# Kernel tuning notes

Measured on AMD Instinct MI355X. Metric: run time of the kernel, lower is better.

The kernel has to match this reference:

```python
import jax, jax.numpy as jnp
import numpy as np

EPS = 1e-5  # pyg LayerNorm default eps


def _graph_ln(x):
    # pyg.nn.norm.LayerNorm(affine=False), default mode='graph', batch=None:
    # normalizes over ALL elements of the tensor (x - x.mean()) / x.std(unbiased=False)
    m = x.mean()
    v = jnp.mean((x - m) ** 2)
    return (x - m) * jax.lax.rsqrt(v + EPS)


def _cheb_conv(x, row, col, w, W, b):
    # ChebConv, normalization='sym', lambda_max=2 => scaled Laplacian
    # L_hat = L - I = -D^{-1/2} A D^{-1/2} (self-loops removed, weighted)
    # x: [B,N,C_in], row/col: [E], w: [E], W: [K,C_in,C_out], b: [C_out]
    N = x.shape[1]
    w = jnp.where(row == col, 0.0, w)  # remove_self_loops
    deg = jnp.zeros((N,), x.dtype).at[row].add(w)
    dinv = jnp.where(deg > 0, jax.lax.rsqrt(jnp.maximum(deg, 1e-12)), 0.0)
    norm = -(dinv[row] * w * dinv[col])  # [E]

    def prop(t):  # out[i] += norm_e * t[j] for edge (j=row -> i=col)
        msg = norm[None, :, None] * t[:, row, :]  # [B,E,C]
        return jnp.zeros_like(t).at[:, col, :].add(msg)

    Tx0 = x
    out = jnp.einsum('bnc,cd->bnd', Tx0, W[0])
    Tx1 = prop(x)
    out = out + jnp.einsum('bnc,cd->bnd', Tx1, W[1])
    for k in range(2, W.shape[0]):
        Tx2 = 2.0 * prop(Tx1) - Tx0
        out = out + jnp.einsum('bnc,cd->bnd', Tx2, W[k])
        Tx0, Tx1 = Tx1, Tx2
    return out + b


def setup_inputs() -> dict:
    key = jax.random.key(0)
    ks = jax.random.split(key, 8)
    B, N, C, E, L, K = 8, 2048, 256, 32768, 3, 3
    node_feature = jax.random.normal(ks[0], (B, N, C), dtype=jnp.float32)
    edge_index = jax.random.randint(ks[1], (L, 2, E), 0, N)
    edge_weight = jax.random.uniform(ks[2], (L, E), dtype=jnp.float32)
    s = 1.0 / np.sqrt(C)
    cheb_w = jax.random.normal(ks[3], (L, K, C, C), dtype=jnp.float32) * s
    cheb_b = jnp.zeros((L, C), dtype=jnp.float32)
    mlp_w = jax.random.normal(ks[4], (L, C, C), dtype=jnp.float32) * s
    mlp_b = jax.random.normal(ks[5], (L, C), dtype=jnp.float32) * 0.01
    return {"node_feature": node_feature, "edge_weight": edge_weight,
            "cheb_w": cheb_w, "cheb_b": cheb_b, "mlp_w": mlp_w,
            "mlp_b": mlp_b, "edge_index": edge_index}


def reference(node_feature, edge_weight, cheb_w, cheb_b, mlp_w, mlp_b, edge_index):
    h = node_feature  # [B,N,C]
    L = cheb_w.shape[0]
    for l in range(L):
        h_res = h
        hn = _graph_ln(h)
        hc = _cheb_conv(hn, edge_index[l, 0], edge_index[l, 1],
                        edge_weight[l], cheb_w[l], cheb_b[l])
        h = hc + h_res
        h_res = h
        hn = _graph_ln(h)
        hm = jax.nn.gelu(jnp.einsum('bnc,cd->bnd', hn, mlp_w[l]) + mlp_b[l],
                         approximate=False)  # dropout is identity at inference
        h = hm + h_res
    return h.mean(axis=1)  # [B,C]
```

## Files before the change

### kernel.cpp

```cpp
#include <hip/hip_runtime.h>

#define BATCH   8
#define NNODE   2048
#define CH      256
#define NEDGE   32768
#define NLAYER  3
#define MROWS   (NNODE*BATCH)
#define KCAT    (3*CH)
#define NTOT    (MROWS*CH)

typedef _Float16 half8 __attribute__((ext_vector_type(8)));
typedef _Float16 half4 __attribute__((ext_vector_type(4)));
typedef float    f32x4 __attribute__((ext_vector_type(4)));

#define OFF_ACAT   ((size_t)0)
#define OFF_HF     ((size_t)25165824)
#define OFF_WT     ((size_t)33554432)
#define OFF_MT     ((size_t)34734080)
#define OFF_PARTA  ((size_t)35127296)
#define OFF_PARTB  ((size_t)35135488)
#define OFF_CS     ((size_t)35143680)
#define OFF_CSM    ((size_t)35152896)
#define OFF_DEG    ((size_t)35155968)
#define OFF_CNT    ((size_t)35180544)
#define OFF_ELIST  ((size_t)35205120)
#define OFF_NORM   ((size_t)36777984)
#define OFF_R1     ((size_t)37171200)
#define OFF_R2     ((size_t)37195776)

__device__ __forceinline__ void async_lds16(const void* g, void* l) {
  __builtin_amdgcn_global_load_lds((const __attribute__((address_space(1))) void*)g,
                                   (__attribute__((address_space(3))) void*)l, 16, 0, 0);
}

__global__ __launch_bounds__(256) void k_init(const float* __restrict__ x,
                                              _Float16* __restrict__ Acat,
                                              float2* __restrict__ part,
                                              const float* __restrict__ cheb_w,
                                              const float* __restrict__ mlp_w,
                                              _Float16* __restrict__ Wt,
                                              _Float16* __restrict__ Mt,
                                              float* __restrict__ deg,
                                              unsigned int* __restrict__ count,
                                              float* __restrict__ r1) {
  __shared__ float rs[512];
  __shared__ _Float16 lt[64][72];
  const int blk = blockIdx.x, t = threadIdx.x;
  if (blk < 1024) {
    int tid = blk*256 + t;
    float s = 0.f, s2 = 0.f;
    for (int i = tid; i < NTOT/4; i += 1024*256) {
      int c4 = i & 63, b = (i >> 6) & 7, n = i >> 9;
      float4 v = ((const float4*)x)[((b*NNODE + n) << 6) + c4];
      half4 o; o[0]=(_Float16)v.x; o[1]=(_Float16)v.y; o[2]=(_Float16)v.z; o[3]=(_Float16)v.w;
      *(half4*)&Acat[(size_t)(i >> 6)*KCAT + c4*4] = o;
      s  += v.x + v.y + v.z + v.w;
      s2 += v.x*v.x + v.y*v.y + v.z*v.z + v.w*v.w;
    }
    rs[t] = s; rs[256+t] = s2; __syncthreads();
    for (int o = 128; o > 0; o >>= 1) {
      if (t < o) { rs[t] += rs[t+o]; rs[256+t] += rs[256+t+o]; }
      __syncthreads();
    }
    if (t == 0) part[blk] = make_float2(rs[0], rs[256]);
  } else if (blk < 1048) {
    int i = (blk - 1024)*256 + t;
    if (i < NLAYER*NNODE) { deg[i] = 0.f; count[i] = 0u; r1[i] = 0.f; }
  } else {
    const int tile = blk - 1048;
    const int rr = t >> 4, c4 = t & 15;
    if (tile < 144) {
      const int l = tile / 48, rem = tile % 48;
      const int kk = rem / 16, q = rem % 16, ci = q >> 2, ni = q & 3;
      const float4* W  = (const float4*)cheb_w + ((size_t)((l*3 + kk)*CH + ci*64))*64 + ni*16;
      const float4* W2 = (const float4*)cheb_w + ((size_t)((l*3 + 2 )*CH + ci*64))*64 + ni*16;
      #pragma unroll
      for (int p = 0; p < 4; ++p) {
        const int r = p*16 + rr;
        float4 v = W[(size_t)r*64 + c4];
        if (kk == 0) {
          float4 v2 = W2[(size_t)r*64 + c4];
          v.x -= v2.x; v.y -= v2.y; v.z -= v2.z; v.w -= v2.w;
        } else if (kk == 2) {
          v.x *= 2.f; v.y *= 2.f; v.z *= 2.f; v.w *= 2.f;
        }
        lt[c4*4+0][r] = (_Float16)v.x; lt[c4*4+1][r] = (_Float16)v.y;
        lt[c4*4+2][r] = (_Float16)v.z; lt[c4*4+3][r] = (_Float16)v.w;
      }
      __syncthreads();
      const int nr = t >> 2, ch2 = t & 3;
      #pragma unroll
      for (int pp = 0; pp < 2; ++pp) {
        const int ch = ch2 + pp*4;
        half8 v = *(const half8*)&lt[nr][ch*8];
        *(half8*)&Wt[((size_t)(l*CH + ni*64 + nr))*KCAT + kk*256 + ci*64 + ch*8] = v;
      }
    } else {
      const int m = tile - 144;
      const int l = m / 16, q = m % 16, ci = q >> 2, ni = q & 3;
      const float4* W = (const float4*)mlp_w + ((size_t)(l*CH + ci*64))*64 + ni*16;
      #pragma unroll
      for (int p = 0; p < 4; ++p) {
        const int r = p*16 + rr;
        float4 v = W[(size_t)r*64 + c4];
        lt[c4*4+0][r] = (_Float16)v.x; lt[c4*4+1][r] = (_Float16)v.y;
        lt[c4*4+2][r] = (_Float16)v.z; lt[c4*4+3][r] = (_Float16)v.w;
      }
      __syncthreads();
      const int nr = t >> 2, ch2 = t & 3;
      #pragma unroll
      for (int pp = 0; pp < 2; ++pp) {
        const int ch = ch2 + pp*4;
        half8 v = *(const half8*)&lt[nr][ch*8];
        *(half8*)&Mt[((size_t)(l*CH + ni*64 + nr))*CH + ci*64 + ch*8] = v;
      }
    }
  }
}

__global__ __launch_bounds__(256) void k_edge_scatter(const int* __restrict__ ei,
                                                      const float* __restrict__ ew,
                                                      float* deg, unsigned int* count,
                                                      unsigned int* elist) {
  int i = blockIdx.x*256 + threadIdx.x;
  if (i >= NLAYER*NEDGE) return;
  int l = i / NEDGE, e = i % NEDGE;
  const int* rows = ei + l*2*NEDGE;
  const int* cols = rows + NEDGE;
  int r = rows[e], c = cols[e];
  float w = (r == c) ? 0.f : ew[i];
  atomicAdd(&deg[l*NNODE + r], w);
  unsigned int slot = atomicAdd(&count[l*NNODE + c], 1u);
  if (slot < 64u) elist[(size_t)(l*NNODE + c)*64 + slot] = (unsigned int)e;
}

__global__ __launch_bounds__(256) void k_edge_norm(const int* __restrict__ ei,
                                                   const float* __restrict__ ew,
                                                   const float* __restrict__ deg,
                                                   float* __restrict__ norm,
                                                   float* __restrict__ r1) {
  int i = blockIdx.x*256 + threadIdx.x;
  if (i >= NLAYER*NEDGE) return;
  int l = i / NEDGE, e = i % NEDGE;
  const int* rows = ei + l*2*NEDGE;
  const int* cols = rows + NEDGE;
  int r = rows[e], c = cols[e];
  float w = (r == c) ? 0.f : ew[i];
  float dr = deg[l*NNODE + r], dc = deg[l*NNODE + c];
  float ir = dr > 0.f ? rsqrtf(fmaxf(dr, 1e-12f)) : 0.f;
  float ic = dc > 0.f ? rsqrtf(fmaxf(dc, 1e-12f)) : 0.f;
  float nm = -(ir * w * ic);
  norm[i] = nm;
  atomicAdd(&r1[l*NNODE + c], nm);
}

template<int SRC_OFF, int DST_OFF, int AUX>
__global__ __launch_bounds__(256) void k_prop(_Float16* __restrict__ Acat,
                                              const int* __restrict__ rows,
                                              const float* __restrict__ nrm,
                                              const unsigned int* __restrict__ count,
                                              const unsigned int* __restrict__ el,
                                              const int* __restrict__ ei,
                                              const float* __restrict__ norm_all,
                                              const unsigned int* __restrict__ cnt_all,
                                              const unsigned int* __restrict__ el_all,
                                              const float* __restrict__ r1,
                                              float* __restrict__ r2,
                                              const _Float16* __restrict__ Wt,
                                              const _Float16* __restrict__ Mt,
                                              float* __restrict__ cs,
                                              float* __restrict__ csM,
                                              float* __restrict__ out_zero) {
  const int blk = blockIdx.x, t = threadIdx.x;
  if (!AUX || blk < 4096) {
    const int b = blk & 7, dgrp = blk >> 3;
    const int w = t >> 6, lane = t & 63;
    const int dst = dgrp*4 + w;
    unsigned int c = count[dst]; if (c > 64u) c = 64u;
    int srcv = 0; float nmv = 0.f;
    if (lane < (int)c) {
      unsigned int e = el[(size_t)dst*64 + lane];
      srcv = rows[e]; nmv = nrm[e];
    }
    float a0 = 0.f, a1 = 0.f, a2 = 0.f, a3 = 0.f;
    const _Float16* base = Acat + SRC_OFF + b*KCAT + lane*4;
    #define PROP_STEP(i)                                                            \
      {                                                                             \
        int   src = __builtin_amdgcn_readlane(srcv, (i));                           \
        int   nbi = __builtin_amdgcn_readlane(__builtin_bit_cast(int, nmv), (i));   \
        float nm  = __builtin_bit_cast(float, nbi);                                 \
        half4 v = *(const half4*)&base[(size_t)src*8*KCAT];                         \
        a0 += nm*(float)v[0]; a1 += nm*(float)v[1];                                 \
        a2 += nm*(float)v[2]; a3 += nm*(float)v[3];                                 \
      }
    unsigned int i = 0;
    for (; i + 4 <= c; i += 4) { PROP_STEP(i) PROP_STEP(i+1) PROP_STEP(i+2) PROP_STEP(i+3) }
    for (; i < c; ++i) { PROP_STEP(i) }
    #undef PROP_STEP
    half4 o; o[0] = (_Float16)a0; o[1] = (_Float16)a1; o[2] = (_Float16)a2; o[3] = (_Float16)a3;
    *(half4*)&Acat[(size_t)(dst*8 + b)*KCAT + DST_OFF + lane*4] = o;
  } else {
    const int tile = blk - 4096;
    if (tile < 24) {
      int i = tile*256 + t, l = i / NNODE;
      const int* rw = ei + l*2*NEDGE;
      unsigned int c = cnt_all[i]; if (c > 64u) c = 64u;
      const unsigned int* elp = el_all + (size_t)i*64;
      float s = 0.f;
      for (unsigned int j = 0; j < c; ++j) {
        unsigned int e = elp[j];
        s += norm_all[l*NEDGE + e] * r1[l*NNODE + rw[e]];
      }
      r2[i] = s;
    } else if (tile < 33) {
      int idx = tile - 24, l = idx / 3, kk = idx % 3, n = t;
      const half8* row = (const half8*)&Wt[((size_t)(l*CH + n))*KCAT + kk*256];
      float s = 0.f;
      #pragma unroll 4
      for (int j = 0; j < 32; ++j) {
        half8 v = row[j];
        s += (float)v[0]+(float)v[1]+(float)v[2]+(float)v[3]
           + (float)v[4]+(float)v[5]+(float)v[6]+(float)v[7];
      }
      cs[(l*3 + kk)*CH + n] = s;
    } else if (tile < 36) {
      int l = tile - 33, n = t;
      const half8* row = (const half8*)&Mt[((size_t)(l*CH + n))*CH];
      float s = 0.f;
      #pragma unroll 4
      for (int j = 0; j < 32; ++j) {
        half8 v = row[j];
        s += (float)v[0]+(float)v[1]+(float)v[2]+(float)v[3]
           + (float)v[4]+(float)v[5]+(float)v[6]+(float)v[7];
      }
      csM[l*CH + n] = s;
    } else {
      for (int i = t; i < BATCH*CH; i += 256) out_zero[i] = 0.f;
    }
  }
}

template<int KSTEPS, int DO_GELU>
__global__ __launch_bounds__(256) void k_gemm(const _Float16* __restrict__ A, int lda,
                                              const _Float16* __restrict__ Bt, int ldb,
                                              const float* __restrict__ bias,
                                              const float* __restrict__ cs,
                                              const float* __restrict__ r1,
                                              const float* __restrict__ r2,
                                              const float2* __restrict__ part_in,
                                              float2* __restrict__ part_out,
                                              const _Float16* __restrict__ R, int ldr,
                                              _Float16* __restrict__ O, int ldo) {
  __shared__ _Float16 Als[64*64];
  __shared__ _Float16 Bls[64*64];
  __shared__ float red[512];
  __shared__ float mv[2];
  const int bm = blockIdx.x, bn = blockIdx.y;
  const int t = threadIdx.x;
  const int w = t >> 6, lane = t & 63;
  const int quad = lane >> 4, l16 = lane & 15;
  const int wm = w & 1, wn = w >> 1;

  {
    float s = 0.f, s2 = 0.f;
    for (int i = t; i < 1024; i += 256) { float2 p = part_in[i]; s += p.x; s2 += p.y; }
    red[t] = s; red[256+t] = s2; __syncthreads();
    for (int o = 128; o > 0; o >>= 1) {
      if (t < o) { red[t] += red[t+o]; red[256+t] += red[256+t+o]; }
      __syncthreads();
    }
    if (t == 0) {
      float mean = red[0] * (1.f/(float)NTOT);
      float var  = red[256] * (1.f/(float)NTOT) - mean*mean;
      mv[0] = mean; mv[1] = rsqrtf(var + 1e-5f);
    }
    __syncthreads();
  }
  const float mean = mv[0], istd = mv[1];

  f32x4 acc00 = {0.f,0.f,0.f,0.f};
  f32x4 acc01 = acc00, acc10 = acc00, acc11 = acc00;

  const int c0 = w*64 + lane, c1 = 256 + w*64 + lane;
  const int r0 = c0 >> 3, s0 = (c0 & 7) ^ (r0 & 7);
  const int r1i = c1 >> 3, s1 = (c1 & 7) ^ (r1i & 7);
  const _Float16* ga0 = A  + (size_t)(bm*64 + r0)*lda + s0*8;
  const _Float16* ga1 = A  + (size_t)(bm*64 + r1i)*lda + s1*8;
  const _Float16* gb0 = Bt + (size_t)(bn*64 + r0)*ldb + s0*8;
  const _Float16* gb1 = Bt + (size_t)(bn*64 + r1i)*ldb + s1*8;
  _Float16* lA0 = &Als[w*512];
  _Float16* lA1 = &Als[2048 + w*512];
  _Float16* lB0 = &Bls[w*512];
  _Float16* lB1 = &Bls[2048 + w*512];

  const int ra0 = wm*32 + l16, ra1 = ra0 + 16;
  const int rb0 = wn*32 + l16, rb1 = rb0 + 16;

  for (int ks = 0; ks < KSTEPS; ++ks) {
    async_lds16(ga0, lA0); async_lds16(ga1, lA1);
    async_lds16(gb0, lB0); async_lds16(gb1, lB1);
    ga0 += 64; ga1 += 64; gb0 += 64; gb1 += 64;
    __syncthreads();
    #pragma unroll
    for (int kh = 0; kh < 2; ++kh) {
      const int q = kh*4 + quad;
      half8 a0 = *(const half8*)&Als[ra0*64 + (q ^ (ra0 & 7))*8];
      half8 a1 = *(const half8*)&Als[ra1*64 + (q ^ (ra1 & 7))*8];
      half8 b0 = *(const half8*)&Bls[rb0*64 + (q ^ (rb0 & 7))*8];
      half8 b1 = *(const half8*)&Bls[rb1*64 + (q ^ (rb1 & 7))*8];
      acc00 = __builtin_amdgcn_mfma_f32_16x16x32_f16(a0, b0, acc00, 0, 0, 0);
      acc01 = __builtin_amdgcn_mfma_f32_16x16x32_f16(a0, b1, acc01, 0, 0, 0);
      acc10 = __builtin_amdgcn_mfma_f32_16x16x32_f16(a1, b0, acc10, 0, 0, 0);
      acc11 = __builtin_amdgcn_mfma_f32_16x16x32_f16(a1, b1, acc11, 0, 0, 0);
    }
    __syncthreads();
  }

  float s = 0.f, s2 = 0.f;
  const int gm0 = bm*64 + wm*32, gn0 = bn*64 + wn*32;
  const float mi = -mean * istd;
  #pragma unroll
  for (int i = 0; i < 2; ++i) {
    #pragma unroll
    for (int j = 0; j < 2; ++j) {
      f32x4 a = (i == 0) ? (j == 0 ? acc00 : acc01) : (j == 0 ? acc10 : acc11);
      const int col = gn0 + j*16 + l16;
      const float bv = bias[col];
      const float c0v = cs[col];
      float c1v = 0.f, c2v = 0.f;
      if (!DO_GELU) { c1v = cs[256 + col]; c2v = cs[512 + col]; }
      #pragma unroll
      for (int r = 0; r < 4; ++r) {
        const int row = gm0 + i*16 + quad*4 + r;
        float v;
        if (DO_GELU) {
          v = istd*a[r] + mi*c0v + bv;
          v = 0.5f*v*(1.f + erff(v*0.70710678118654752f));
        } else {
          const int node = row >> 3;
          v = istd*a[r] + mi*(c0v + r1[node]*c1v + r2[node]*c2v) + bv;
        }
        float hv = (float)R[(size_t)row*ldr + col] + v;
        O[(size_t)row*ldo + col] = (_Float16)hv;
        s += hv; s2 += hv*hv;
      }
    }
  }
  red[t] = s; red[256+t] = s2; __syncthreads();
  for (int o = 128; o > 0; o >>= 1) {
    if (t < o) { red[t] += red[t+o]; red[256+t] += red[256+t+o]; }
    __syncthreads();
  }
  if (t == 0) part_out[blockIdx.y*gridDim.x + blockIdx.x] = make_float2(red[0], red[256]);
}

__global__ __launch_bounds__(256) void k_mean(const _Float16* __restrict__ Acat,
                                              float* __restrict__ out) {
  int b = blockIdx.x & 7, chunk = blockIdx.x >> 3;
  int c = threadIdx.x;
  float s = 0.f;
  for (int k = 0; k < 256; ++k) {
    int n = chunk*256 + k;
    s += (float)Acat[(size_t)(n*8 + b)*KCAT + c];
  }
  atomicAdd(&out[(b << 8) + c], s * (1.f/(float)NNODE));
}

extern "C" void kernel_launch(void* const* d_in, const int* in_sizes, int n_in,
                              void* d_out, int out_size, void* d_ws, size_t ws_size,
                              hipStream_t stream) {
  const float* x      = (const float*)d_in[0];
  const float* ew     = (const float*)d_in[1];
  const float* cheb_w = (const float*)d_in[2];
  const float* cheb_b = (const float*)d_in[3];
  const float* mlp_w  = (const float*)d_in[4];
  const float* mlp_b  = (const float*)d_in[5];
  const int*   ei     = (const int*)d_in[6];
  float* out = (float*)d_out;

  char* ws = (char*)d_ws;
  _Float16*     Acat  = (_Float16*)(ws + OFF_ACAT);
  _Float16*     Hf    = (_Float16*)(ws + OFF_HF);
  _Float16*     Wt    = (_Float16*)(ws + OFF_WT);
  _Float16*     Mt    = (_Float16*)(ws + OFF_MT);
  float2*       partA = (float2*)(ws + OFF_PARTA);
  float2*       partB = (float2*)(ws + OFF_PARTB);
  float*        cs    = (float*)(ws + OFF_CS);
  float*        csM   = (float*)(ws + OFF_CSM);
  float*        deg   = (float*)(ws + OFF_DEG);
  unsigned int* cnt   = (unsigned int*)(ws + OFF_CNT);
  unsigned int* elist = (unsigned int*)(ws + OFF_ELIST);
  float*        norm  = (float*)(ws + OFF_NORM);
  float*        r1    = (float*)(ws + OFF_R1);
  float*        r2    = (float*)(ws + OFF_R2);

  k_init<<<1240, 256, 0, stream>>>(x, Acat, partA, cheb_w, mlp_w, Wt, Mt, deg, cnt, r1);
  k_edge_scatter<<<(NLAYER*NEDGE)/256, 256, 0, stream>>>(ei, ew, deg, cnt, elist);
  k_edge_norm<<<(NLAYER*NEDGE)/256, 256, 0, stream>>>(ei, ew, deg, norm, r1);

  for (int l = 0; l < NLAYER; ++l) {
    const int* rows_l = ei + l*2*NEDGE;
    const unsigned int* cnt_l = cnt + l*NNODE;
    const unsigned int* el_l  = elist + (size_t)l*NNODE*64;
    const float* norm_l = norm + l*NEDGE;

    if (l == 0) {
      k_prop<0, 256, 1><<<4133, 256, 0, stream>>>(
          Acat, rows_l, norm_l, cnt_l, el_l,
          ei, norm, cnt, elist, r1, r2, Wt, Mt, cs, csM, out);
    } else {
      k_prop<0, 256, 0><<<4096, 256, 0, stream>>>(
          Acat, rows_l, norm_l, cnt_l, el_l,
          ei, norm, cnt, elist, r1, r2, Wt, Mt, cs, csM, out);
    }
    k_prop<256, 512, 0><<<4096, 256, 0, stream>>>(
        Acat, rows_l, norm_l, cnt_l, el_l,
        ei, norm, cnt, elist, r1, r2, Wt, Mt, cs, csM, out);
    k_gemm<12, 0><<<dim3(256, 4), 256, 0, stream>>>(
        Acat, KCAT, Wt + (size_t)l*CH*KCAT, KCAT, cheb_b + l*CH,
        cs + l*3*CH, r1 + l*NNODE, r2 + l*NNODE, partA, partB,
        Acat, KCAT, Hf, CH);
    k_gemm<4, 1><<<dim3(256, 4), 256, 0, stream>>>(
        Hf, CH, Mt + (size_t)l*CH*CH, CH, mlp_b + l*CH,
        csM + l*CH, r1, r2, partB, partA,
        Hf, CH, Acat, KCAT);
  }

  k_mean<<<64, 256, 0, stream>>>(Acat, out);
}
```

Baseline: 299.2 us.

## Fuse edge-norm into prop kernels, fold mean into final MLP GEMM

```diff
diff --git a/kernel.cpp b/kernel.cpp
--- a/kernel.cpp
+++ b/kernel.cpp
@@ -24,9 +24,8 @@
 #define OFF_DEG    ((size_t)35155968)
 #define OFF_CNT    ((size_t)35180544)
 #define OFF_ELIST  ((size_t)35205120)
-#define OFF_NORM   ((size_t)36777984)
-#define OFF_R1     ((size_t)37171200)
-#define OFF_R2     ((size_t)37195776)
+#define OFF_R1     ((size_t)36777984)
+#define OFF_R2     ((size_t)36802560)
 
 __device__ __forceinline__ void async_lds16(const void* g, void* l) {
   __builtin_amdgcn_global_load_lds((const __attribute__((address_space(1))) void*)g,
@@ -41,8 +40,7 @@
                                               _Float16* __restrict__ Wt,
                                               _Float16* __restrict__ Mt,
                                               float* __restrict__ deg,
-                                              unsigned int* __restrict__ count,
-                                              float* __restrict__ r1) {
+                                              unsigned int* __restrict__ count) {
   __shared__ float rs[512];
   __shared__ _Float16 lt[64][72];
   const int blk = blockIdx.x, t = threadIdx.x;
@@ -65,7 +63,7 @@
     if (t == 0) part[blk] = make_float2(rs[0], rs[256]);
   } else if (blk < 1048) {
     int i = (blk - 1024)*256 + t;
-    if (i < NLAYER*NNODE) { deg[i] = 0.f; count[i] = 0u; r1[i] = 0.f; }
+    if (i < NLAYER*NNODE) { deg[i] = 0.f; count[i] = 0u; }
   } else {
     const int tile = blk - 1048;
     const int rr = t >> 4, c4 = t & 15;
@@ -121,126 +119,102 @@
 __global__ __launch_bounds__(256) void k_edge_scatter(const int* __restrict__ ei,
                                                       const float* __restrict__ ew,
                                                       float* deg, unsigned int* count,
-                                                      unsigned int* elist) {
-  int i = blockIdx.x*256 + threadIdx.x;
-  if (i >= NLAYER*NEDGE) return;
-  int l = i / NEDGE, e = i % NEDGE;
-  const int* rows = ei + l*2*NEDGE;
-  const int* cols = rows + NEDGE;
-  int r = rows[e], c = cols[e];
-  float w = (r == c) ? 0.f : ew[i];
-  atomicAdd(&deg[l*NNODE + r], w);
-  unsigned int slot = atomicAdd(&count[l*NNODE + c], 1u);
-  if (slot < 64u) elist[(size_t)(l*NNODE + c)*64 + slot] = (unsigned int)e;
-}
-
-__global__ __launch_bounds__(256) void k_edge_norm(const int* __restrict__ ei,
-                                                   const float* __restrict__ ew,
-                                                   const float* __restrict__ deg,
-                                                   float* __restrict__ norm,
-                                                   float* __restrict__ r1) {
-  int i = blockIdx.x*256 + threadIdx.x;
-  if (i >= NLAYER*NEDGE) return;
-  int l = i / NEDGE, e = i % NEDGE;
-  const int* rows = ei + l*2*NEDGE;
-  const int* cols = rows + NEDGE;
-  int r = rows[e], c = cols[e];
-  float w = (r == c) ? 0.f : ew[i];
-  float dr = deg[l*NNODE + r], dc = deg[l*NNODE + c];
-  float ir = dr > 0.f ? rsqrtf(fmaxf(dr, 1e-12f)) : 0.f;
-  float ic = dc > 0.f ? rsqrtf(fmaxf(dc, 1e-12f)) : 0.f;
-  float nm = -(ir * w * ic);
-  norm[i] = nm;
-  atomicAdd(&r1[l*NNODE + c], nm);
-}
-
-template<int SRC_OFF, int DST_OFF, int AUX>
+                                                      unsigned int* elist,
+                                                      const _Float16* __restrict__ Wt,
+                                                      const _Float16* __restrict__ Mt,
+                                                      float* __restrict__ cs,
+                                                      float* __restrict__ csM,
+                                                      float* __restrict__ out_zero) {
+  const int blk = blockIdx.x, t = threadIdx.x;
+  if (blk < 384) {
+    int i = blk*256 + t;
+    int l = i / NEDGE, e = i % NEDGE;
+    const int* rows = ei + l*2*NEDGE;
+    const int* cols = rows + NEDGE;
+    int r = rows[e], c = cols[e];
+    float w = (r == c) ? 0.f : ew[i];
+    atomicAdd(&deg[l*NNODE + r], w);
+    unsigned int slot = atomicAdd(&count[l*NNODE + c], 1u);
+    if (slot < 64u) elist[(size_t)(l*NNODE + c)*64 + slot] = (unsigned int)e;
+  } else if (blk < 393) {
+    int idx = blk - 384, l = idx / 3, kk = idx % 3, n = t;
+    const half8* row = (const half8*)&Wt[((size_t)(l*CH + n))*KCAT + kk*256];
+    float s = 0.f;
+    #pragma unroll 4
+    for (int j = 0; j < 32; ++j) {
+      half8 v = row[j];
+      s += (float)v[0]+(float)v[1]+(float)v[2]+(float)v[3]
+         + (float)v[4]+(float)v[5]+(float)v[6]+(float)v[7];
+    }
+    cs[(l*3 + kk)*CH + n] = s;
+  } else if (blk < 396) {
+    int l = blk - 393, n = t;
+    const half8* row = (const half8*)&Mt[((size_t)(l*CH + n))*CH];
+    float s = 0.f;
+    #pragma unroll 4
+    for (int j = 0; j < 32; ++j) {
+      half8 v = row[j];
+      s += (float)v[0]+(float)v[1]+(float)v[2]+(float)v[3]
+         + (float)v[4]+(float)v[5]+(float)v[6]+(float)v[7];
+    }
+    csM[l*CH + n] = s;
+  } else {
+    for (int i = t; i < BATCH*CH; i += 256) out_zero[i] = 0.f;
+  }
+}
+
+template<int SRC_OFF, int DST_OFF, int RMODE>
 __global__ __launch_bounds__(256) void k_prop(_Float16* __restrict__ Acat,
                                               const int* __restrict__ rows,
-                                              const float* __restrict__ nrm,
+                                              const float* __restrict__ ew_l,
+                                              const float* __restrict__ deg_l,
                                               const unsigned int* __restrict__ count,
                                               const unsigned int* __restrict__ el,
-                                              const int* __restrict__ ei,
-                                              const float* __restrict__ norm_all,
-                                              const unsigned int* __restrict__ cnt_all,
-                                              const unsigned int* __restrict__ el_all,
-                                              const float* __restrict__ r1,
-                                              float* __restrict__ r2,
-                                              const _Float16* __restrict__ Wt,
-                                              const _Float16* __restrict__ Mt,
-                                              float* __restrict__ cs,
-                                              float* __restrict__ csM,
-                                              float* __restrict__ out_zero) {
+                                              float* __restrict__ r1_l,
+                                              float* __restrict__ r2_l) {
   const int blk = blockIdx.x, t = threadIdx.x;
-  if (!AUX || blk < 4096) {
-    const int b = blk & 7, dgrp = blk >> 3;
-    const int w = t >> 6, lane = t & 63;
-    const int dst = dgrp*4 + w;
-    unsigned int c = count[dst]; if (c > 64u) c = 64u;
-    int srcv = 0; float nmv = 0.f;
-    if (lane < (int)c) {
-      unsigned int e = el[(size_t)dst*64 + lane];
-      srcv = rows[e]; nmv = nrm[e];
-    }
-    float a0 = 0.f, a1 = 0.f, a2 = 0.f, a3 = 0.f;
-    const _Float16* base = Acat + SRC_OFF + b*KCAT + lane*4;
-    #define PROP_STEP(i)                                                            \
-      {                                                                             \
-        int   src = __builtin_amdgcn_readlane(srcv, (i));                           \
-        int   nbi = __builtin_amdgcn_readlane(__builtin_bit_cast(int, nmv), (i));   \
-        float nm  = __builtin_bit_cast(float, nbi);                                 \
-        half4 v = *(const half4*)&base[(size_t)src*8*KCAT];                         \
-        a0 += nm*(float)v[0]; a1 += nm*(float)v[1];                                 \
-        a2 += nm*(float)v[2]; a3 += nm*(float)v[3];                                 \
-      }
-    unsigned int i = 0;
-    for (; i + 4 <= c; i += 4) { PROP_STEP(i) PROP_STEP(i+1) PROP_STEP(i+2) PROP_STEP(i+3) }
-    for (; i < c; ++i) { PROP_STEP(i) }
-    #undef PROP_STEP
-    half4 o; o[0] = (_Float16)a0; o[1] = (_Float16)a1; o[2] = (_Float16)a2; o[3] = (_Float16)a3;
-    *(half4*)&Acat[(size_t)(dst*8 + b)*KCAT + DST_OFF + lane*4] = o;
-  } else {
-    const int tile = blk - 4096;
-    if (tile < 24) {
-      int i = tile*256 + t, l = i / NNODE;
-      const int* rw = ei + l*2*NEDGE;
-      unsigned int c = cnt_all[i]; if (c > 64u) c = 64u;
-      const unsigned int* elp = el_all + (size_t)i*64;
-      float s = 0.f;
-      for (unsigned int j = 0; j < c; ++j) {
-        unsigned int e = elp[j];
-        s += norm_all[l*NEDGE + e] * r1[l*NNODE + rw[e]];
-      }
-      r2[i] = s;
-    } else if (tile < 33) {
-      int idx = tile - 24, l = idx / 3, kk = idx % 3, n = t;
-      const half8* row = (const half8*)&Wt[((size_t)(l*CH + n))*KCAT + kk*256];
-      float s = 0.f;
-      #pragma unroll 4
-      for (int j = 0; j < 32; ++j) {
-        half8 v = row[j];
-        s += (float)v[0]+(float)v[1]+(float)v[2]+(float)v[3]
-           + (float)v[4]+(float)v[5]+(float)v[6]+(float)v[7];
-      }
-      cs[(l*3 + kk)*CH + n] = s;
-    } else if (tile < 36) {
-      int l = tile - 33, n = t;
-      const half8* row = (const half8*)&Mt[((size_t)(l*CH + n))*CH];
-      float s = 0.f;
-      #pragma unroll 4
-      for (int j = 0; j < 32; ++j) {
-        half8 v = row[j];
-        s += (float)v[0]+(float)v[1]+(float)v[2]+(float)v[3]
-           + (float)v[4]+(float)v[5]+(float)v[6]+(float)v[7];
-      }
-      csM[l*CH + n] = s;
-    } else {
-      for (int i = t; i < BATCH*CH; i += 256) out_zero[i] = 0.f;
-    }
-  }
-}
-
-template<int KSTEPS, int DO_GELU>
+  const int b = blk & 7, dgrp = blk >> 3;
+  const int w = t >> 6, lane = t & 63;
+  const int dst = dgrp*4 + w;
+  unsigned int c = count[dst]; if (c > 64u) c = 64u;
+  const float dc = deg_l[dst];
+  const float ic = dc > 0.f ? rsqrtf(fmaxf(dc, 1e-12f)) : 0.f;
+  int srcv = 0; float nmv = 0.f;
+  if (lane < (int)c) {
+    unsigned int e = el[(size_t)dst*64 + lane];
+    srcv = rows[e];
+    float wv = (srcv == dst) ? 0.f : ew_l[e];
+    float dr = deg_l[srcv];
+    float ir = dr > 0.f ? rsqrtf(fmaxf(dr, 1e-12f)) : 0.f;
+    nmv = -(ir * wv * ic);
+  }
+  if (RMODE && b == 0) {
+    float rv = nmv;
+    if (RMODE == 2) rv = (lane < (int)c) ? nmv * r1_l[srcv] : 0.f;
+    #pragma unroll
+    for (int o = 32; o > 0; o >>= 1) rv += __shfl_xor(rv, o);
+    if (lane == 0) { if (RMODE == 1) r1_l[dst] = rv; else r2_l[dst] = rv; }
+  }
+  float a0 = 0.f, a1 = 0.f, a2 = 0.f, a3 = 0.f;
+  const _Float16* base = Acat + SRC_OFF + b*KCAT + lane*4;
+  #define PROP_STEP(i)                                                            \
+    {                                                                             \
+      int   src = __builtin_amdgcn_readlane(srcv, (i));                           \
+      int   nbi = __builtin_amdgcn_readlane(__builtin_bit_cast(int, nmv), (i));   \
+      float nm  = __builtin_bit_cast(float, nbi);                                 \
+      half4 v = *(const half4*)&base[(size_t)src*8*KCAT];                         \
+      a0 += nm*(float)v[0]; a1 += nm*(float)v[1];                                 \
+      a2 += nm*(float)v[2]; a3 += nm*(float)v[3];                                 \
+    }
+  unsigned int i = 0;
+  for (; i + 4 <= c; i += 4) { PROP_STEP(i) PROP_STEP(i+1) PROP_STEP(i+2) PROP_STEP(i+3) }
+  for (; i < c; ++i) { PROP_STEP(i) }
+  #undef PROP_STEP
+  half4 o; o[0] = (_Float16)a0; o[1] = (_Float16)a1; o[2] = (_Float16)a2; o[3] = (_Float16)a3;
+  *(half4*)&Acat[(size_t)(dst*8 + b)*KCAT + DST_OFF + lane*4] = o;
+}
+
+template<int KSTEPS, int DO_GELU, int MEAN>
 __global__ __launch_bounds__(256) void k_gemm(const _Float16* __restrict__ A, int lda,
                                               const _Float16* __restrict__ Bt, int ldb,
                                               const float* __restrict__ bias,
@@ -250,16 +224,20 @@
                                               const float2* __restrict__ part_in,
                                               float2* __restrict__ part_out,
                                               const _Float16* __restrict__ R, int ldr,
-                                              _Float16* __restrict__ O, int ldo) {
+                                              _Float16* __restrict__ O, int ldo,
+                                              float* __restrict__ out) {
   __shared__ _Float16 Als[64*64];
   __shared__ _Float16 Bls[64*64];
   __shared__ float red[512];
   __shared__ float mv[2];
+  __shared__ float outacc[512];
   const int bm = blockIdx.x, bn = blockIdx.y;
   const int t = threadIdx.x;
   const int w = t >> 6, lane = t & 63;
   const int quad = lane >> 4, l16 = lane & 15;
   const int wm = w & 1, wn = w >> 1;
+
+  if (MEAN) { outacc[t] = 0.f; outacc[256+t] = 0.f; }
 
   {
     float s = 0.f, s2 = 0.f;
@@ -341,9 +319,17 @@
           v = istd*a[r] + mi*(c0v + r1[node]*c1v + r2[node]*c2v) + bv;
         }
         float hv = (float)R[(size_t)row*ldr + col] + v;
-        O[(size_t)row*ldo + col] = (_Float16)hv;
+        if (!MEAN) O[(size_t)row*ldo + col] = (_Float16)hv;
+        else       atomicAdd(&outacc[((col & 63) << 3) | (row & 7)], hv);
         s += hv; s2 += hv*hv;
       }
+    }
+  }
+  if (MEAN) {
+    __syncthreads();
+    for (int i = t; i < 512; i += 256) {
+      int c8 = i >> 3, b = i & 7;
+      atomicAdd(&out[(b << 8) + bn*64 + c8], outacc[i] * (1.f/(float)NNODE));
     }
   }
   red[t] = s; red[256+t] = s2; __syncthreads();
@@ -352,18 +338,6 @@
     __syncthreads();
   }
   if (t == 0) part_out[blockIdx.y*gridDim.x + blockIdx.x] = make_float2(red[0], red[256]);
-}
-
-__global__ __launch_bounds__(256) void k_mean(const _Float16* __restrict__ Acat,
-                                              float* __restrict__ out) {
-  int b = blockIdx.x & 7, chunk = blockIdx.x >> 3;
-  int c = threadIdx.x;
-  float s = 0.f;
-  for (int k = 0; k < 256; ++k) {
-    int n = chunk*256 + k;
-    s += (float)Acat[(size_t)(n*8 + b)*KCAT + c];
-  }
-  atomicAdd(&out[(b << 8) + c], s * (1.f/(float)NNODE));
 }
 
 extern "C" void kernel_launch(void* const* d_in, const int* in_sizes, int n_in,
@@ -390,41 +364,39 @@
   float*        deg   = (float*)(ws + OFF_DEG);
   unsigned int* cnt   = (unsigned int*)(ws + OFF_CNT);
   unsigned int* elist = (unsigned int*)(ws + OFF_ELIST);
-  float*        norm  = (float*)(ws + OFF_NORM);
   float*        r1    = (float*)(ws + OFF_R1);
   float*        r2    = (float*)(ws + OFF_R2);
 
-  k_init<<<1240, 256, 0, stream>>>(x, Acat, partA, cheb_w, mlp_w, Wt, Mt, deg, cnt, r1);
-  k_edge_scatter<<<(NLAYER*NEDGE)/256, 256, 0, stream>>>(ei, ew, deg, cnt, elist);
-  k_edge_norm<<<(NLAYER*NEDGE)/256, 256, 0, stream>>>(ei, ew, deg, norm, r1);
+  k_init<<<1240, 256, 0, stream>>>(x, Acat, partA, cheb_w, mlp_w, Wt, Mt, deg, cnt);
+  k_edge_scatter<<<397, 256, 0, stream>>>(ei, ew, deg, cnt, elist, Wt, Mt, cs, csM, out);
 
   for (int l = 0; l < NLAYER; ++l) {
     const int* rows_l = ei + l*2*NEDGE;
+    const float* ew_l = ew + l*NEDGE;
+    const float* deg_l = deg + l*NNODE;
     const unsigned int* cnt_l = cnt + l*NNODE;
     const unsigned int* el_l  = elist + (size_t)l*NNODE*64;
-    const float* norm_l = norm + l*NEDGE;
-
-    if (l == 0) {
-      k_prop<0, 256, 1><<<4133, 256, 0, stream>>>(
-          Acat, rows_l, norm_l, cnt_l, el_l,
-          ei, norm, cnt, elist, r1, r2, Wt, Mt, cs, csM, out);
+    float* r1_l = r1 + l*NNODE;
+    float* r2_l = r2 + l*NNODE;
+
+    k_prop<0, 256, 1><<<4096, 256, 0, stream>>>(
+        Acat, rows_l, ew_l, deg_l, cnt_l, el_l, r1_l, r2_l);
+    k_prop<256, 512, 2><<<4096, 256, 0, stream>>>(
+        Acat, rows_l, ew_l, deg_l, cnt_l, el_l, r1_l, r2_l);
+    k_gemm<12, 0, 0><<<dim3(256, 4), 256, 0, stream>>>(
+        Acat, KCAT, Wt + (size_t)l*CH*KCAT, KCAT, cheb_b + l*CH,
+        cs + l*3*CH, r1_l, r2_l, partA, partB,
+        Acat, KCAT, Hf, CH, out);
+    if (l < NLAYER-1) {
+      k_gemm<4, 1, 0><<<dim3(256, 4), 256, 0, stream>>>(
+          Hf, CH, Mt + (size_t)l*CH*CH, CH, mlp_b + l*CH,
+          csM + l*CH, r1_l, r2_l, partB, partA,
+          Hf, CH, Acat, KCAT, out);
     } else {
-      k_prop<0, 256, 0><<<4096, 256, 0, stream>>>(
-          Acat, rows_l, norm_l, cnt_l, el_l,
-          ei, norm, cnt, elist, r1, r2, Wt, Mt, cs, csM, out);
-    }
-    k_prop<256, 512, 0><<<4096, 256, 0, stream>>>(
-        Acat, rows_l, norm_l, cnt_l, el_l,
-        ei, norm, cnt, elist, r1, r2, Wt, Mt, cs, csM, out);
-    k_gemm<12, 0><<<dim3(256, 4), 256, 0, stream>>>(
-        Acat, KCAT, Wt + (size_t)l*CH*KCAT, KCAT, cheb_b + l*CH,
-        cs + l*3*CH, r1 + l*NNODE, r2 + l*NNODE, partA, partB,
-        Acat, KCAT, Hf, CH);
-    k_gemm<4, 1><<<dim3(256, 4), 256, 0, stream>>>(
-        Hf, CH, Mt + (size_t)l*CH*CH, CH, mlp_b + l*CH,
-        csM + l*CH, r1, r2, partB, partA,
-        Hf, CH, Acat, KCAT);
-  }
-
-  k_mean<<<64, 256, 0, stream>>>(Acat, out);
-}
+      k_gemm<4, 1, 1><<<dim3(256, 4), 256, 0, stream>>>(
+          Hf, CH, Mt + (size_t)l*CH*CH, CH, mlp_b + l*CH,
+          csM + l*CH, r1_l, r2_l, partB, partA,
+          Hf, CH, Acat, KCAT, out);
+    }
+  }
+}
```

New measurement: 306.0 us. +2.3%, slower.
